# Kernel optimization log

Hardware: AMD Instinct MI355X
Metric: run time of the kernel (lower is better)

Reference implementation:

```python
import jax, jax.numpy as jnp
import numpy as np

TEMPERATURE = 8.0  # sqrt(d_k) with d_k = 64


def setup_inputs() -> dict:
    key = jax.random.key(0)
    k1, k2, k3, k4 = jax.random.split(key, 4)
    B, S, D = 16, 2048, 64  # B = batch * n_heads
    q = jax.random.normal(k1, (B, S, D), dtype=jnp.float32)
    k = jax.random.normal(k2, (B, S, D), dtype=jnp.float32)
    v = jax.random.normal(k3, (B, S, D), dtype=jnp.float32)
    # boolean mask: True = masked out. Low prob so no row is fully masked.
    mask = jax.random.uniform(k4, (B, S, S)) < 0.1
    return {"q": q, "k": k, "v": v, "mask": mask}


def reference(q, k, v, mask):
    # attn = (q @ k^T) / temperature, masked_fill(mask, -inf), softmax over last dim
    attn = jnp.einsum("bqd,bkd->bqk", q, k) / TEMPERATURE
    attn = jnp.where(mask, -jnp.inf, attn)
    attn = jax.nn.softmax(attn, axis=2)
    output = jnp.einsum("bqk,bkd->bqd", attn, v)
    return output, attn
```

## Files before the change

### kernel.cpp

```cpp
#include <hip/hip_runtime.h>

typedef _Float16 half8 __attribute__((ext_vector_type(8)));
typedef _Float16 half4 __attribute__((ext_vector_type(4)));
typedef float    floatx4 __attribute__((ext_vector_type(4)));

#define NB  16
#define SEQ 2048
#define DIM 64

#define MFMA32(a,b,c) __builtin_amdgcn_mfma_f32_16x16x32_f16((a),(b),(c),0,0,0)
#define MFMA16(a,b,c) __builtin_amdgcn_mfma_f32_16x16x16f16((a),(b),(c),0,0,0)

__global__ __launch_bounds__(256) void cvt_qk_kernel(const float* __restrict__ q,
                                                     const float* __restrict__ k,
                                                     _Float16* __restrict__ qh,
                                                     _Float16* __restrict__ kh) {
    size_t i = ((size_t)blockIdx.x * 256 + threadIdx.x) * 4;
    float4 a = *(const float4*)(q + i);
    float4 b = *(const float4*)(k + i);
    half4 ha = { (_Float16)a.x, (_Float16)a.y, (_Float16)a.z, (_Float16)a.w };
    half4 hb = { (_Float16)b.x, (_Float16)b.y, (_Float16)b.z, (_Float16)b.w };
    *(half4*)(qh + i) = ha;
    *(half4*)(kh + i) = hb;
}

__global__ __launch_bounds__(256) void cvt_vt_kernel(const float* __restrict__ v,
                                                     _Float16* __restrict__ vt) {
    __shared__ float tile[64][65];
    const int b  = blockIdx.x >> 5;
    const int s0 = (blockIdx.x & 31) << 6;
    const int t  = threadIdx.x;
    {
        const int row = t >> 2;
        const int c0  = (t & 3) << 4;
        const float* src = v + ((size_t)(b * SEQ + s0 + row)) * DIM + c0;
        #pragma unroll
        for (int i = 0; i < 4; ++i) {
            float4 x = *(const float4*)(src + i * 4);
            tile[row][c0 + i*4 + 0] = x.x;
            tile[row][c0 + i*4 + 1] = x.y;
            tile[row][c0 + i*4 + 2] = x.z;
            tile[row][c0 + i*4 + 3] = x.w;
        }
    }
    __syncthreads();
    {
        const int d  = t >> 2;
        const int sb = (t & 3) << 4;
        _Float16* dst = vt + ((size_t)(b * DIM + d)) * SEQ + s0 + sb;
        #pragma unroll
        for (int i = 0; i < 4; ++i) {
            half4 h = { (_Float16)tile[sb + i*4 + 0][d],
                        (_Float16)tile[sb + i*4 + 1][d],
                        (_Float16)tile[sb + i*4 + 2][d],
                        (_Float16)tile[sb + i*4 + 3][d] };
            *(half4*)(dst + i*4) = h;
        }
    }
}

__global__ __launch_bounds__(256) void mask_bits_kernel(const int* __restrict__ mask,
                                                        unsigned int* __restrict__ bits) {
    const int wave = threadIdx.x >> 6;
    const int lane = threadIdx.x & 63;
    const size_t row = (size_t)blockIdx.x * 4 + wave;
    const int* mp = mask + row * SEQ + lane;
    unsigned int keep = 0;
    #pragma unroll
    for (int it = 0; it < 32; ++it) {
        int m = __builtin_nontemporal_load(mp + it * 64);
        unsigned long long bal = __ballot(m != 0);
        unsigned int half = (lane & 1) ? (unsigned int)(bal >> 32) : (unsigned int)bal;
        if ((lane >> 1) == it) keep = half;
    }
    bits[row * 64 + lane] = keep;
}

__global__ __launch_bounds__(256, 8) void attn_kernel(
    const _Float16* __restrict__ qh, const _Float16* __restrict__ kh,
    const _Float16* __restrict__ vt, const unsigned int* __restrict__ bits,
    float* __restrict__ out, float* __restrict__ attn)
{
    __shared__ float wsum[4][16];
    __shared__ __align__(16) float outred[4][16][68];

    const int blk  = ((blockIdx.x & 7) << 8) + (blockIdx.x >> 3);
    const int b    = blk >> 7;
    const int r0   = (blk & 127) << 4;
    const int lane = threadIdx.x & 63;
    const int wave = threadIdx.x >> 6;
    const int rl   = lane & 15;
    const int g    = lane >> 4;

    const size_t qoff = ((size_t)(b * SEQ + r0 + rl)) * DIM + g * 8;
    const half8 qa0 = *(const half8*)(qh + qoff);
    const half8 qa1 = *(const half8*)(qh + qoff + 32);

    const _Float16* kbase = kh + (size_t)b * SEQ * DIM + (size_t)rl * DIM + g * 8;
    const _Float16* vbase = vt + ((size_t)b * DIM + rl) * SEQ + g * 4;
    const unsigned int* bbase = bits + ((size_t)(b * SEQ + r0 + rl)) * 64 + wave;

    float rs = 0.f;
    unsigned int pb = bbase[0];

    for (int cc = 0; cc < 16; ++cc) {
        const int jj = (cc * 4 + wave) * 32;
        const unsigned int bm = pb;
        if (cc < 15) pb = bbase[(cc + 1) * 4];
        const _Float16* kp = kbase + (size_t)jj * DIM;
        half8 ka0 = *(const half8*)(kp);
        half8 ka1 = *(const half8*)(kp + 32);
        half8 kb0 = *(const half8*)(kp + 16 * DIM);
        half8 kb1 = *(const half8*)(kp + 16 * DIM + 32);
        floatx4 c0 = {0.f,0.f,0.f,0.f}, c1 = {0.f,0.f,0.f,0.f};
        c0 = MFMA32(ka0, qa0, c0);
        c0 = MFMA32(ka1, qa1, c0);
        c1 = MFMA32(kb0, qa0, c1);
        c1 = MFMA32(kb1, qa1, c1);
        const unsigned int blo = bm >> (g * 4);
        const unsigned int bhi = bm >> (g * 4 + 16);
        float e0 = (blo & 1u) ? 0.f : __expf(c0[0] * 0.125f);
        float e1 = (blo & 2u) ? 0.f : __expf(c0[1] * 0.125f);
        float e2 = (blo & 4u) ? 0.f : __expf(c0[2] * 0.125f);
        float e3 = (blo & 8u) ? 0.f : __expf(c0[3] * 0.125f);
        float e4 = (bhi & 1u) ? 0.f : __expf(c1[0] * 0.125f);
        float e5 = (bhi & 2u) ? 0.f : __expf(c1[1] * 0.125f);
        float e6 = (bhi & 4u) ? 0.f : __expf(c1[2] * 0.125f);
        float e7 = (bhi & 8u) ? 0.f : __expf(c1[3] * 0.125f);
        rs += (e0 + e1) + (e2 + e3) + (e4 + e5) + (e6 + e7);
    }

    rs += __shfl_xor(rs, 16);
    rs += __shfl_xor(rs, 32);
    if (g == 0) wsum[wave][rl] = rs;
    __syncthreads();
    const float inv = 1.0f / (wsum[0][rl] + wsum[1][rl] + wsum[2][rl] + wsum[3][rl]);

    floatx4 o0 = {0.f,0.f,0.f,0.f}, o1 = {0.f,0.f,0.f,0.f};
    floatx4 o2 = {0.f,0.f,0.f,0.f}, o3 = {0.f,0.f,0.f,0.f};
    float* abase = attn + ((size_t)(b * SEQ + r0 + rl)) * SEQ + g * 4;

    for (int cc = 0; cc < 16; ++cc) {
        const int jj = (cc * 4 + wave) * 32;
        const unsigned int bm = bbase[cc * 4];
        const _Float16* kp = kbase + (size_t)jj * DIM;
        half8 ka0 = *(const half8*)(kp);
        half8 ka1 = *(const half8*)(kp + 32);
        half8 kb0 = *(const half8*)(kp + 16 * DIM);
        half8 kb1 = *(const half8*)(kp + 16 * DIM + 32);
        floatx4 c0 = {0.f,0.f,0.f,0.f}, c1 = {0.f,0.f,0.f,0.f};
        c0 = MFMA32(ka0, qa0, c0);
        c0 = MFMA32(ka1, qa1, c0);
        c1 = MFMA32(kb0, qa0, c1);
        c1 = MFMA32(kb1, qa1, c1);

        const unsigned int blo = bm >> (g * 4);
        const unsigned int bhi = bm >> (g * 4 + 16);
        float e0 = (blo & 1u) ? 0.f : __expf(c0[0] * 0.125f);
        float e1 = (blo & 2u) ? 0.f : __expf(c0[1] * 0.125f);
        float e2 = (blo & 4u) ? 0.f : __expf(c0[2] * 0.125f);
        float e3 = (blo & 8u) ? 0.f : __expf(c0[3] * 0.125f);
        float e4 = (bhi & 1u) ? 0.f : __expf(c1[0] * 0.125f);
        float e5 = (bhi & 2u) ? 0.f : __expf(c1[1] * 0.125f);
        float e6 = (bhi & 4u) ? 0.f : __expf(c1[2] * 0.125f);
        float e7 = (bhi & 8u) ? 0.f : __expf(c1[3] * 0.125f);

        floatx4 a0 = { e0 * inv, e1 * inv, e2 * inv, e3 * inv };
        floatx4 a1 = { e4 * inv, e5 * inv, e6 * inv, e7 * inv };
        *(floatx4*)(abase + jj)      = a0;
        *(floatx4*)(abase + jj + 16) = a1;

        half4 h0 = { (_Float16)e0, (_Float16)e1, (_Float16)e2, (_Float16)e3 };
        half4 h1 = { (_Float16)e4, (_Float16)e5, (_Float16)e6, (_Float16)e7 };

        const _Float16* vp = vbase + jj;
        half4 va00 = *(const half4*)(vp);
        half4 va01 = *(const half4*)(vp + 16);
        half4 va10 = *(const half4*)(vp + 16 * SEQ);
        half4 va11 = *(const half4*)(vp + 16 * SEQ + 16);
        half4 va20 = *(const half4*)(vp + 32 * SEQ);
        half4 va21 = *(const half4*)(vp + 32 * SEQ + 16);
        half4 va30 = *(const half4*)(vp + 48 * SEQ);
        half4 va31 = *(const half4*)(vp + 48 * SEQ + 16);
        o0 = MFMA16(va00, h0, o0);
        o0 = MFMA16(va01, h1, o0);
        o1 = MFMA16(va10, h0, o1);
        o1 = MFMA16(va11, h1, o1);
        o2 = MFMA16(va20, h0, o2);
        o2 = MFMA16(va21, h1, o2);
        o3 = MFMA16(va30, h0, o3);
        o3 = MFMA16(va31, h1, o3);
    }

    {
        float* orow = &outred[wave][rl][g * 4];
        *(floatx4*)(orow +  0) = o0;
        *(floatx4*)(orow + 16) = o1;
        *(floatx4*)(orow + 32) = o2;
        *(floatx4*)(orow + 48) = o3;
    }
    __syncthreads();
    {
        const int r  = threadIdx.x >> 4;
        const int c4 = (threadIdx.x & 15) << 2;
        floatx4 s0 = *(const floatx4*)(&outred[0][r][c4]);
        floatx4 s1 = *(const floatx4*)(&outred[1][r][c4]);
        floatx4 s2 = *(const floatx4*)(&outred[2][r][c4]);
        floatx4 s3 = *(const floatx4*)(&outred[3][r][c4]);
        floatx4 s = (s0 + s1) + (s2 + s3);
        const float inv2 = 1.0f / (wsum[0][r] + wsum[1][r] + wsum[2][r] + wsum[3][r]);
        floatx4 ov = { s[0] * inv2, s[1] * inv2, s[2] * inv2, s[3] * inv2 };
        *(floatx4*)(out + ((size_t)(b * SEQ + r0 + r)) * DIM + c4) = ov;
    }
}

extern "C" void kernel_launch(void* const* d_in, const int* in_sizes, int n_in,
                              void* d_out, int out_size, void* d_ws, size_t ws_size,
                              hipStream_t stream) {
    const float* q = (const float*)d_in[0];
    const float* k = (const float*)d_in[1];
    const float* v = (const float*)d_in[2];
    const int* mask = (const int*)d_in[3];

    float* out  = (float*)d_out;
    float* attn = out + (size_t)NB * SEQ * DIM;

    _Float16* qh = (_Float16*)d_ws;
    _Float16* kh = qh + (size_t)NB * SEQ * DIM;
    _Float16* vt = kh + (size_t)NB * SEQ * DIM;
    unsigned int* bits = (unsigned int*)(vt + (size_t)NB * SEQ * DIM);

    cvt_qk_kernel<<<(NB * SEQ * DIM) / 1024, 256, 0, stream>>>(q, k, qh, kh);
    cvt_vt_kernel<<<NB * (SEQ / 64), 256, 0, stream>>>(v, vt);
    mask_bits_kernel<<<(NB * SEQ) / 4, 256, 0, stream>>>(mask, bits);
    attn_kernel<<<NB * (SEQ / 16), 256, 0, stream>>>(qh, kh, vt, bits, out, attn);
}
```

Before: 670.2 us.

## Software-pipeline K/V/mask loads in attention loops and batch mask loads

```diff
diff --git a/kernel.cpp b/kernel.cpp
--- a/kernel.cpp
+++ b/kernel.cpp
@@ -65,18 +65,21 @@
     const int lane = threadIdx.x & 63;
     const size_t row = (size_t)blockIdx.x * 4 + wave;
     const int* mp = mask + row * SEQ + lane;
+    int m[32];
+    #pragma unroll
+    for (int it = 0; it < 32; ++it)
+        m[it] = __builtin_nontemporal_load(mp + it * 64);
     unsigned int keep = 0;
     #pragma unroll
     for (int it = 0; it < 32; ++it) {
-        int m = __builtin_nontemporal_load(mp + it * 64);
-        unsigned long long bal = __ballot(m != 0);
+        unsigned long long bal = __ballot(m[it] != 0);
         unsigned int half = (lane & 1) ? (unsigned int)(bal >> 32) : (unsigned int)bal;
         if ((lane >> 1) == it) keep = half;
     }
     bits[row * 64 + lane] = keep;
 }
 
-__global__ __launch_bounds__(256, 8) void attn_kernel(
+__global__ __launch_bounds__(256, 4) void attn_kernel(
     const _Float16* __restrict__ qh, const _Float16* __restrict__ kh,
     const _Float16* __restrict__ vt, const unsigned int* __restrict__ bits,
     float* __restrict__ out, float* __restrict__ attn)
@@ -102,32 +105,42 @@
 
     float rs = 0.f;
     unsigned int pb = bbase[0];
-
-    for (int cc = 0; cc < 16; ++cc) {
-        const int jj = (cc * 4 + wave) * 32;
-        const unsigned int bm = pb;
-        if (cc < 15) pb = bbase[(cc + 1) * 4];
-        const _Float16* kp = kbase + (size_t)jj * DIM;
+    {
+        const _Float16* kp = kbase + (size_t)(wave * 32) * DIM;
         half8 ka0 = *(const half8*)(kp);
         half8 ka1 = *(const half8*)(kp + 32);
         half8 kb0 = *(const half8*)(kp + 16 * DIM);
         half8 kb1 = *(const half8*)(kp + 16 * DIM + 32);
-        floatx4 c0 = {0.f,0.f,0.f,0.f}, c1 = {0.f,0.f,0.f,0.f};
-        c0 = MFMA32(ka0, qa0, c0);
-        c0 = MFMA32(ka1, qa1, c0);
-        c1 = MFMA32(kb0, qa0, c1);
-        c1 = MFMA32(kb1, qa1, c1);
-        const unsigned int blo = bm >> (g * 4);
-        const unsigned int bhi = bm >> (g * 4 + 16);
-        float e0 = (blo & 1u) ? 0.f : __expf(c0[0] * 0.125f);
-        float e1 = (blo & 2u) ? 0.f : __expf(c0[1] * 0.125f);
-        float e2 = (blo & 4u) ? 0.f : __expf(c0[2] * 0.125f);
-        float e3 = (blo & 8u) ? 0.f : __expf(c0[3] * 0.125f);
-        float e4 = (bhi & 1u) ? 0.f : __expf(c1[0] * 0.125f);
-        float e5 = (bhi & 2u) ? 0.f : __expf(c1[1] * 0.125f);
-        float e6 = (bhi & 4u) ? 0.f : __expf(c1[2] * 0.125f);
-        float e7 = (bhi & 8u) ? 0.f : __expf(c1[3] * 0.125f);
-        rs += (e0 + e1) + (e2 + e3) + (e4 + e5) + (e6 + e7);
+
+        for (int cc = 0; cc < 16; ++cc) {
+            const int jn = (((cc + 1) * 4 + wave) * 32) & (SEQ - 1);
+            const _Float16* kn = kbase + (size_t)jn * DIM;
+            half8 na0 = *(const half8*)(kn);
+            half8 na1 = *(const half8*)(kn + 32);
+            half8 nb0 = *(const half8*)(kn + 16 * DIM);
+            half8 nb1 = *(const half8*)(kn + 16 * DIM + 32);
+            const unsigned int bm = pb;
+            pb = bbase[((cc + 1) * 4) & 63];
+
+            floatx4 c0 = {0.f,0.f,0.f,0.f}, c1 = {0.f,0.f,0.f,0.f};
+            c0 = MFMA32(ka0, qa0, c0);
+            c0 = MFMA32(ka1, qa1, c0);
+            c1 = MFMA32(kb0, qa0, c1);
+            c1 = MFMA32(kb1, qa1, c1);
+            const unsigned int blo = bm >> (g * 4);
+            const unsigned int bhi = bm >> (g * 4 + 16);
+            float e0 = (blo & 1u) ? 0.f : __expf(c0[0] * 0.125f);
+            float e1 = (blo & 2u) ? 0.f : __expf(c0[1] * 0.125f);
+            float e2 = (blo & 4u) ? 0.f : __expf(c0[2] * 0.125f);
+            float e3 = (blo & 8u) ? 0.f : __expf(c0[3] * 0.125f);
+            float e4 = (bhi & 1u) ? 0.f : __expf(c1[0] * 0.125f);
+            float e5 = (bhi & 2u) ? 0.f : __expf(c1[1] * 0.125f);
+            float e6 = (bhi & 4u) ? 0.f : __expf(c1[2] * 0.125f);
+            float e7 = (bhi & 8u) ? 0.f : __expf(c1[3] * 0.125f);
+            rs += (e0 + e1) + (e2 + e3) + (e4 + e5) + (e6 + e7);
+
+            ka0 = na0; ka1 = na1; kb0 = nb0; kb1 = nb1;
+        }
     }
 
     rs += __shfl_xor(rs, 16);
@@ -140,40 +153,13 @@
     floatx4 o2 = {0.f,0.f,0.f,0.f}, o3 = {0.f,0.f,0.f,0.f};
     float* abase = attn + ((size_t)(b * SEQ + r0 + rl)) * SEQ + g * 4;
 
-    for (int cc = 0; cc < 16; ++cc) {
-        const int jj = (cc * 4 + wave) * 32;
-        const unsigned int bm = bbase[cc * 4];
-        const _Float16* kp = kbase + (size_t)jj * DIM;
+    {
+        const _Float16* kp = kbase + (size_t)(wave * 32) * DIM;
         half8 ka0 = *(const half8*)(kp);
         half8 ka1 = *(const half8*)(kp + 32);
         half8 kb0 = *(const half8*)(kp + 16 * DIM);
         half8 kb1 = *(const half8*)(kp + 16 * DIM + 32);
-        floatx4 c0 = {0.f,0.f,0.f,0.f}, c1 = {0.f,0.f,0.f,0.f};
-        c0 = MFMA32(ka0, qa0, c0);
-        c0 = MFMA32(ka1, qa1, c0);
-        c1 = MFMA32(kb0, qa0, c1);
-        c1 = MFMA32(kb1, qa1, c1);
-
-        const unsigned int blo = bm >> (g * 4);
-        const unsigned int bhi = bm >> (g * 4 + 16);
-        float e0 = (blo & 1u) ? 0.f : __expf(c0[0] * 0.125f);
-        float e1 = (blo & 2u) ? 0.f : __expf(c0[1] * 0.125f);
-        float e2 = (blo & 4u) ? 0.f : __expf(c0[2] * 0.125f);
-        float e3 = (blo & 8u) ? 0.f : __expf(c0[3] * 0.125f);
-        float e4 = (bhi & 1u) ? 0.f : __expf(c1[0] * 0.125f);
-        float e5 = (bhi & 2u) ? 0.f : __expf(c1[1] * 0.125f);
-        float e6 = (bhi & 4u) ? 0.f : __expf(c1[2] * 0.125f);
-        float e7 = (bhi & 8u) ? 0.f : __expf(c1[3] * 0.125f);
-
-        floatx4 a0 = { e0 * inv, e1 * inv, e2 * inv, e3 * inv };
-        floatx4 a1 = { e4 * inv, e5 * inv, e6 * inv, e7 * inv };
-        *(floatx4*)(abase + jj)      = a0;
-        *(floatx4*)(abase + jj + 16) = a1;
-
-        half4 h0 = { (_Float16)e0, (_Float16)e1, (_Float16)e2, (_Float16)e3 };
-        half4 h1 = { (_Float16)e4, (_Float16)e5, (_Float16)e6, (_Float16)e7 };
-
-        const _Float16* vp = vbase + jj;
+        const _Float16* vp = vbase + wave * 32;
         half4 va00 = *(const half4*)(vp);
         half4 va01 = *(const half4*)(vp + 16);
         half4 va10 = *(const half4*)(vp + 16 * SEQ);
@@ -182,14 +168,65 @@
         half4 va21 = *(const half4*)(vp + 32 * SEQ + 16);
         half4 va30 = *(const half4*)(vp + 48 * SEQ);
         half4 va31 = *(const half4*)(vp + 48 * SEQ + 16);
-        o0 = MFMA16(va00, h0, o0);
-        o0 = MFMA16(va01, h1, o0);
-        o1 = MFMA16(va10, h0, o1);
-        o1 = MFMA16(va11, h1, o1);
-        o2 = MFMA16(va20, h0, o2);
-        o2 = MFMA16(va21, h1, o2);
-        o3 = MFMA16(va30, h0, o3);
-        o3 = MFMA16(va31, h1, o3);
+        unsigned int bm = bbase[0];
+
+        for (int cc = 0; cc < 16; ++cc) {
+            const int jj = (cc * 4 + wave) * 32;
+            const int jn = (((cc + 1) * 4 + wave) * 32) & (SEQ - 1);
+            const _Float16* kn = kbase + (size_t)jn * DIM;
+            half8 na0 = *(const half8*)(kn);
+            half8 na1 = *(const half8*)(kn + 32);
+            half8 nb0 = *(const half8*)(kn + 16 * DIM);
+            half8 nb1 = *(const half8*)(kn + 16 * DIM + 32);
+            const _Float16* vn = vbase + jn;
+            half4 wa00 = *(const half4*)(vn);
+            half4 wa01 = *(const half4*)(vn + 16);
+            half4 wa10 = *(const half4*)(vn + 16 * SEQ);
+            half4 wa11 = *(const half4*)(vn + 16 * SEQ + 16);
+            half4 wa20 = *(const half4*)(vn + 32 * SEQ);
+            half4 wa21 = *(const half4*)(vn + 32 * SEQ + 16);
+            half4 wa30 = *(const half4*)(vn + 48 * SEQ);
+            half4 wa31 = *(const half4*)(vn + 48 * SEQ + 16);
+            const unsigned int bmn = bbase[((cc + 1) * 4) & 63];
+
+            floatx4 c0 = {0.f,0.f,0.f,0.f}, c1 = {0.f,0.f,0.f,0.f};
+            c0 = MFMA32(ka0, qa0, c0);
+            c0 = MFMA32(ka1, qa1, c0);
+            c1 = MFMA32(kb0, qa0, c1);
+            c1 = MFMA32(kb1, qa1, c1);
+
+            const unsigned int blo = bm >> (g * 4);
+            const unsigned int bhi = bm >> (g * 4 + 16);
+            float e0 = (blo & 1u) ? 0.f : __expf(c0[0] * 0.125f);
+            float e1 = (blo & 2u) ? 0.f : __expf(c0[1] * 0.125f);
+            float e2 = (blo & 4u) ? 0.f : __expf(c0[2] * 0.125f);
+            float e3 = (blo & 8u) ? 0.f : __expf(c0[3] * 0.125f);
+            float e4 = (bhi & 1u) ? 0.f : __expf(c1[0] * 0.125f);
+            float e5 = (bhi & 2u) ? 0.f : __expf(c1[1] * 0.125f);
+            float e6 = (bhi & 4u) ? 0.f : __expf(c1[2] * 0.125f);
+            float e7 = (bhi & 8u) ? 0.f : __expf(c1[3] * 0.125f);
+
+            half4 h0 = { (_Float16)e0, (_Float16)e1, (_Float16)e2, (_Float16)e3 };
+            half4 h1 = { (_Float16)e4, (_Float16)e5, (_Float16)e6, (_Float16)e7 };
+            o0 = MFMA16(va00, h0, o0);
+            o0 = MFMA16(va01, h1, o0);
+            o1 = MFMA16(va10, h0, o1);
+            o1 = MFMA16(va11, h1, o1);
+            o2 = MFMA16(va20, h0, o2);
+            o2 = MFMA16(va21, h1, o2);
+            o3 = MFMA16(va30, h0, o3);
+            o3 = MFMA16(va31, h1, o3);
+
+            floatx4 a0 = { e0 * inv, e1 * inv, e2 * inv, e3 * inv };
+            floatx4 a1 = { e4 * inv, e5 * inv, e6 * inv, e7 * inv };
+            *(floatx4*)(abase + jj)      = a0;
+            *(floatx4*)(abase + jj + 16) = a1;
+
+            ka0 = na0; ka1 = na1; kb0 = nb0; kb1 = nb1;
+            va00 = wa00; va01 = wa01; va10 = wa10; va11 = wa11;
+            va20 = wa20; va21 = wa21; va30 = wa30; va31 = wa31;
+            bm = bmn;
+        }
     }
 
     {
```

Result: no change. 680.5 us (+1.5%).
